# Kernel optimization log

Measured on AMD Instinct MI355X. Metric: run time of the kernel, lower is better.

Reference implementation:

```python
import jax, jax.numpy as jnp
import numpy as np

N, D, E, OUT = 100000, 128, 600000, 128


def setup_inputs() -> dict:
    key = jax.random.key(0)
    k1, k2, k3, k4, k5 = jax.random.split(key, 5)
    x = jax.random.normal(k1, (N, D), dtype=jnp.float32)
    # Linear params (stored as [in, out]; y = h @ W + b, same math as nn.Linear)
    W = jax.random.normal(k2, (D, OUT), dtype=jnp.float32) * (1.0 / np.sqrt(D))
    b = jax.random.normal(k3, (OUT,), dtype=jnp.float32) * 0.01
    # Flattened ragged neighbor lists as COO edges: node edge_dst[e] aggregates x[edge_src[e]]
    edge_src = jax.random.randint(k4, (E,), 0, N, dtype=jnp.int32)
    edge_dst = jnp.sort(jax.random.randint(k5, (E,), 0, N, dtype=jnp.int32))
    return {"x": x, "W": W, "b": b, "edge_src": edge_src, "edge_dst": edge_dst}


def reference(x, W, b, edge_src, edge_dst):
    n = x.shape[0]
    # segment-mean of neighbor features per destination node
    neigh_sum = jax.ops.segment_sum(x[edge_src], edge_dst, num_segments=n)  # [N, D]
    deg = jax.ops.segment_sum(jnp.ones((edge_dst.shape[0],), x.dtype), edge_dst, num_segments=n)  # [N]
    # nodes with no neighbors keep zero mean (matches `if neigh:` branch)
    neigh_mean = neigh_sum / jnp.maximum(deg, 1.0)[:, None]
    h = x + neigh_mean
    return jax.nn.relu(h @ W + b)
```

## Files before the change

kernel.cpp:

```cpp
#include <hip/hip_runtime.h>
#include <hip/hip_bf16.h>


#define FD  128
#define BR  32
#define BRF 64
#define HSB 136

typedef __attribute__((ext_vector_type(8))) short bf16x8;
typedef __attribute__((ext_vector_type(4))) float f32x4;

__device__ __forceinline__ short f2bf(float f) {
    unsigned u = __float_as_uint(f);
    return (short)((u + 0x7FFFu + ((u >> 16) & 1u)) >> 16);
}
__device__ __forceinline__ float bf2f(short s) {
    return __uint_as_float(((unsigned)(unsigned short)s) << 16);
}

__global__ __launch_bounds__(256) void prep_full_kernel(
    const float* __restrict__ x, const float* __restrict__ W,
    const int* __restrict__ edst, int* __restrict__ rp,
    short* __restrict__ pkW, short* __restrict__ xb, int N, int E)
{
    const int gid = blockIdx.x * 256 + threadIdx.x;
    const int nth = gridDim.x * 256;

    const int nv = N * FD / 8;
    for (int i = gid; i < nv; i += nth) {
        float4 f0 = *(const float4*)(x + (size_t)i * 8);
        float4 f1 = *(const float4*)(x + (size_t)i * 8 + 4);
        short tmp[8] = {f2bf(f0.x), f2bf(f0.y), f2bf(f0.z), f2bf(f0.w),
                        f2bf(f1.x), f2bf(f1.y), f2bf(f1.z), f2bf(f1.w)};
        *(bf16x8*)(xb + (size_t)i * 8) = *(bf16x8*)tmp;
    }
    for (int e = gid; e < E; e += nth) {
        int cur = edst[e];
        int prev = e ? edst[e - 1] : -1;
        for (int v = prev + 1; v <= cur; ++v) rp[v] = e;
        if (e == E - 1)
            for (int v = cur + 1; v <= N; ++v) rp[v] = E;
    }
    if (E == 0) {
        for (int v = gid; v <= N; v += nth) rp[v] = 0;
    }
    if (gid < 2048) {
        int wave = gid >> 9, rem = gid & 511;
        int ct = rem >> 8, rem2 = rem & 255;
        int kt = rem2 >> 6, lane = rem2 & 63;
        int q = lane >> 4, lr = lane & 15;
        int col = wave * 32 + ct * 16 + lr;
        int k0 = kt * 32 + q * 8;
        short tmp[8];
#pragma unroll
        for (int e2 = 0; e2 < 8; ++e2)
            tmp[e2] = f2bf(W[(size_t)(k0 + e2) * FD + col]);
        *(bf16x8*)(pkW + (size_t)gid * 8) = *(bf16x8*)tmp;
    }
}

__device__ __forceinline__ void issue8(const short* __restrict__ xb, int srcv,
                                       int qb, int ql, int j0, int m, uint4 v[8])
{
#pragma unroll
    for (int u = 0; u < 8; ++u) {
        int jj = j0 + u;
        int idx = __shfl(srcv, qb + (jj & 15));
        if (jj >= m) idx = 0;
        v[u] = *(const uint4*)(xb + (size_t)idx * FD + 8 * ql);
    }
}

__device__ __forceinline__ void acc8(const uint4 v[8], int c, float2 a[4])
{
#pragma unroll
    for (int u = 0; u < 8; ++u) {
        float f = (u < c) ? 1.f : 0.f;
        unsigned w;
        w = v[u].x;
        a[0].x = fmaf(__uint_as_float(w << 16), f, a[0].x);
        a[0].y = fmaf(__uint_as_float(w & 0xFFFF0000u), f, a[0].y);
        w = v[u].y;
        a[1].x = fmaf(__uint_as_float(w << 16), f, a[1].x);
        a[1].y = fmaf(__uint_as_float(w & 0xFFFF0000u), f, a[1].y);
        w = v[u].z;
        a[2].x = fmaf(__uint_as_float(w << 16), f, a[2].x);
        a[2].y = fmaf(__uint_as_float(w & 0xFFFF0000u), f, a[2].y);
        w = v[u].w;
        a[3].x = fmaf(__uint_as_float(w << 16), f, a[3].x);
        a[3].y = fmaf(__uint_as_float(w & 0xFFFF0000u), f, a[3].y);
    }
}

__device__ __forceinline__ void row_tail(const short* __restrict__ xb,
                                         const int* __restrict__ esrc,
                                         int s, int e, int srcv,
                                         int qb, int ql, float2 a[4])
{
    int deg = e - s;
    if (deg > 8) {
        uint4 v2[8];
        int m16 = deg < 16 ? deg : 16;
        issue8(xb, srcv, qb, ql, 8, m16, v2);
        acc8(v2, m16 - 8, a);
        for (int cs = s + 16; cs < e; cs += 16) {
            int m = e - cs; if (m > 16) m = 16;
            int sv = (cs + ql < e) ? esrc[cs + ql] : 0;
            for (int j0 = 0; j0 < m; j0 += 8) {
                issue8(xb, sv, qb, ql, j0, m, v2);
                int c = m - j0; if (c > 8) c = 8;
                acc8(v2, c, a);
            }
        }
    }
}

__device__ __forceinline__ void finalize_row(short* shb, int rb, int ql,
                                             const bf16x8 xv, const float2 a[4], int deg)
{
    float inv = 1.0f / (float)(deg > 0 ? deg : 1);
    short hb[8];
#pragma unroll
    for (int k = 0; k < 4; ++k) {
        hb[2 * k]     = f2bf(bf2f(xv[2 * k])     + a[k].x * inv);
        hb[2 * k + 1] = f2bf(bf2f(xv[2 * k + 1]) + a[k].y * inv);
    }
    *(bf16x8*)(shb + rb * HSB + 8 * ql) = *(bf16x8*)hb;
}

__global__ __launch_bounds__(256) void meanagg_main3_kernel(
    const short* __restrict__ xb, const short* __restrict__ pkW,
    const float* __restrict__ bias, const int* __restrict__ esrc,
    const int* __restrict__ rp, float* __restrict__ out, int N, int E)
{
    __shared__ short shb[BR * HSB];
    __shared__ int seg[BR + 1];

    const int t = threadIdx.x;
    const int base = blockIdx.x * BR;

    if (t < BR + 1) {
        int idx = base + t;
        seg[t] = rp[idx > N ? N : idx];
    }
    __syncthreads();

    const int wave = t >> 6;
    const int lane = t & 63;
    const int qw = lane >> 4;
    const int ql = lane & 15;
    const int qb = qw << 4;

    const int rb0 = wave * 8 + qw;
    const int rb1 = rb0 + 4;
    const int r0 = base + rb0, r1 = base + rb1;

    const int s0 = seg[rb0], e0 = seg[rb0 + 1];
    const int s1 = seg[rb1], e1 = seg[rb1 + 1];

    int srcv0 = (s0 + ql < e0) ? esrc[s0 + ql] : 0;
    int srcv1 = (s1 + ql < e1) ? esrc[s1 + ql] : 0;
    bf16x8 xv0 = {0, 0, 0, 0, 0, 0, 0, 0}, xv1 = xv0;
    if (r0 < N) xv0 = *(const bf16x8*)(xb + (size_t)r0 * FD + 8 * ql);
    if (r1 < N) xv1 = *(const bf16x8*)(xb + (size_t)r1 * FD + 8 * ql);

    const int deg0 = e0 - s0, deg1 = e1 - s1;
    const int m0 = deg0 < 16 ? deg0 : 16;
    const int m1 = deg1 < 16 ? deg1 : 16;

    uint4 v0[8], v1[8];
    issue8(xb, srcv0, qb, ql, 0, m0, v0);
    issue8(xb, srcv1, qb, ql, 0, m1, v1);

    float2 a[4] = {{0.f, 0.f}, {0.f, 0.f}, {0.f, 0.f}, {0.f, 0.f}};
    acc8(v0, m0 < 8 ? m0 : 8, a);
    row_tail(xb, esrc, s0, e0, srcv0, qb, ql, a);
    finalize_row(shb, rb0, ql, xv0, a, deg0);

    a[0] = a[1] = a[2] = a[3] = make_float2(0.f, 0.f);
    acc8(v1, m1 < 8 ? m1 : 8, a);
    row_tail(xb, esrc, s1, e1, srcv1, qb, ql, a);
    finalize_row(shb, rb1, ql, xv1, a, deg1);

    __syncthreads();

    const int lr = lane & 15;
    const int q  = lane >> 4;
    const int colb = wave * 32;

    bf16x8 bfr[2][4];
#pragma unroll
    for (int ct = 0; ct < 2; ++ct)
#pragma unroll
        for (int kt = 0; kt < 4; ++kt) {
            int f = ((wave * 2 + ct) * 4 + kt) * 64 + lane;
            bfr[ct][kt] = *(const bf16x8*)(pkW + (size_t)f * 8);
        }

    f32x4 acc[2][2];
#pragma unroll
    for (int rt = 0; rt < 2; ++rt) {
        acc[rt][0] = (f32x4){0.f, 0.f, 0.f, 0.f};
        acc[rt][1] = (f32x4){0.f, 0.f, 0.f, 0.f};
    }

#pragma unroll
    for (int rt = 0; rt < 2; ++rt)
#pragma unroll
        for (int kt = 0; kt < 4; ++kt) {
            bf16x8 av = *(const bf16x8*)(shb + (rt * 16 + lr) * HSB + kt * 32 + q * 8);
            acc[rt][0] = __builtin_amdgcn_mfma_f32_16x16x32_bf16(av, bfr[0][kt], acc[rt][0], 0, 0, 0);
            acc[rt][1] = __builtin_amdgcn_mfma_f32_16x16x32_bf16(av, bfr[1][kt], acc[rt][1], 0, 0, 0);
        }

    const float b0 = bias[colb + lr];
    const float b1 = bias[colb + 16 + lr];

#pragma unroll
    for (int rt = 0; rt < 2; ++rt)
#pragma unroll
        for (int j = 0; j < 4; ++j) {
            int row = base + rt * 16 + q * 4 + j;
            if (row < N) {
                float o0 = acc[rt][0][j] + b0; o0 = o0 > 0.f ? o0 : 0.f;
                float o1 = acc[rt][1][j] + b1; o1 = o1 > 0.f ? o1 : 0.f;
                out[(size_t)row * FD + colb + lr]      = o0;
                out[(size_t)row * FD + colb + 16 + lr] = o1;
            }
        }
}

__global__ __launch_bounds__(256) void prep_kernel(
    const float* __restrict__ W, const int* __restrict__ edst,
    int* __restrict__ rp, short* __restrict__ pkW, int N, int E)
{
    int gid = blockIdx.x * 256 + threadIdx.x;
    if (gid < E) {
        int cur = edst[gid];
        int prev = gid ? edst[gid - 1] : -1;
        for (int v = prev + 1; v <= cur; ++v) rp[v] = gid;
        if (gid == E - 1)
            for (int v = cur + 1; v <= N; ++v) rp[v] = E;
    }
    if (gid < 2048) {
        int wave = gid >> 9, rem = gid & 511;
        int ct = rem >> 8, rem2 = rem & 255;
        int kt = rem2 >> 6, lane = rem2 & 63;
        int q = lane >> 4, lr = lane & 15;
        int col = wave * 32 + ct * 16 + lr;
        int k0 = kt * 32 + q * 8;
        short tmp[8];
#pragma unroll
        for (int e = 0; e < 8; ++e)
            tmp[e] = f2bf(W[(size_t)(k0 + e) * FD + col]);
        *(bf16x8*)(pkW + (size_t)gid * 8) = *(bf16x8*)tmp;
    }
}

__global__ __launch_bounds__(256) void meanagg_main_kernel(
    const float* __restrict__ x, const short* __restrict__ pkW,
    const float* __restrict__ bias, const int* __restrict__ esrc,
    const int* __restrict__ rp, float* __restrict__ out, int N, int E)
{
    __shared__ short shb[BRF * HSB];
    __shared__ int seg[BRF + 1];

    const int t = threadIdx.x;
    const int base = blockIdx.x * BRF;

    if (t < BRF + 1) {
        int idx = base + t;
        seg[t] = rp[idx > N ? N : idx];
    }
    __syncthreads();

    const int wave = t >> 6;
    const int lane = t & 63;
    const int sw = lane >> 5;
    const int sl = lane & 31;
    const int lb = sw << 5;
    const int rowbase = wave * 16;

    for (int it = 0; it < 8; ++it) {
        int cur_rb = rowbase + it * 2 + sw;
        int cur_r  = base + cur_rb;
        if (cur_r >= N) break;
        int cur_s = seg[cur_rb], cur_e = seg[cur_rb + 1];
        float4 a0 = make_float4(0.f, 0.f, 0.f, 0.f), a1 = a0;
        for (int cs = cur_s; cs < cur_e; cs += 32) {
            int m = cur_e - cs; if (m > 32) m = 32;
            int srcv = (cs + sl < cur_e) ? esrc[cs + sl] : 0;
            for (int j0 = 0; j0 < m; j0 += 8) {
                const int rem = m - j0;
#pragma unroll
                for (int u = 0; u < 8; ++u) {
                    int idx = __shfl(srcv, lb + ((j0 + u) & 31));
                    float4 v = *(const float4*)(x + (size_t)idx * FD + 4 * sl);
                    float f = (u < rem) ? 1.f : 0.f;
                    float4* A = (u & 1) ? &a1 : &a0;
                    A->x = fmaf(v.x, f, A->x);
                    A->y = fmaf(v.y, f, A->y);
                    A->z = fmaf(v.z, f, A->z);
                    A->w = fmaf(v.w, f, A->w);
                }
            }
        }
        float4 xv = *(const float4*)(x + (size_t)cur_r * FD + 4 * sl);
        int deg = cur_e - cur_s;
        float inv = 1.0f / (float)(deg > 0 ? deg : 1);
        short4 hb;
        hb.x = f2bf(xv.x + (a0.x + a1.x) * inv);
        hb.y = f2bf(xv.y + (a0.y + a1.y) * inv);
        hb.z = f2bf(xv.z + (a0.z + a1.z) * inv);
        hb.w = f2bf(xv.w + (a0.w + a1.w) * inv);
        *(short4*)(shb + cur_rb * HSB + 4 * sl) = hb;
    }
    __syncthreads();

    const int lr = lane & 15;
    const int q  = lane >> 4;
    const int colb = wave * 32;

    bf16x8 bfr[2][4];
#pragma unroll
    for (int ct = 0; ct < 2; ++ct)
#pragma unroll
        for (int kt = 0; kt < 4; ++kt) {
            int f = ((wave * 2 + ct) * 4 + kt) * 64 + lane;
            bfr[ct][kt] = *(const bf16x8*)(pkW + (size_t)f * 8);
        }

    f32x4 acc[4][2];
#pragma unroll
    for (int rt = 0; rt < 4; ++rt) {
        acc[rt][0] = (f32x4){0.f, 0.f, 0.f, 0.f};
        acc[rt][1] = (f32x4){0.f, 0.f, 0.f, 0.f};
    }

#pragma unroll
    for (int rt = 0; rt < 4; ++rt)
#pragma unroll
        for (int kt = 0; kt < 4; ++kt) {
            bf16x8 av = *(const bf16x8*)(shb + (rt * 16 + lr) * HSB + kt * 32 + q * 8);
            acc[rt][0] = __builtin_amdgcn_mfma_f32_16x16x32_bf16(av, bfr[0][kt], acc[rt][0], 0, 0, 0);
            acc[rt][1] = __builtin_amdgcn_mfma_f32_16x16x32_bf16(av, bfr[1][kt], acc[rt][1], 0, 0, 0);
        }

    const float b0 = bias[colb + lr];
    const float b1 = bias[colb + 16 + lr];

#pragma unroll
    for (int rt = 0; rt < 4; ++rt)
#pragma unroll
        for (int j = 0; j < 4; ++j) {
            int row = base + rt * 16 + q * 4 + j;
            if (row < N) {
                float v0 = acc[rt][0][j] + b0; v0 = v0 > 0.f ? v0 : 0.f;
                float v1 = acc[rt][1][j] + b1; v1 = v1 > 0.f ? v1 : 0.f;
                out[(size_t)row * FD + colb + lr]      = v0;
                out[(size_t)row * FD + colb + 16 + lr] = v1;
            }
        }
}

__global__ __launch_bounds__(256) void meanagg_fused_kernel(
    const float* __restrict__ x, const float* __restrict__ W,
    const float* __restrict__ bias, const int* __restrict__ esrc,
    const int* __restrict__ edst, float* __restrict__ out, int N, int E)
{
    __shared__ short shb[BRF * HSB];
    __shared__ int seg[BRF + 1];

    const int t = threadIdx.x;
    const int base = blockIdx.x * BRF;

    if (t < BRF + 1) {
        int v = base + t;
        int lo = 0, hi = E;
        while (lo < hi) {
            int mid = (lo + hi) >> 1;
            if (edst[mid] < v) lo = mid + 1; else hi = mid;
        }
        seg[t] = lo;
    }
    __syncthreads();

    const int wave = t >> 6;
    const int lane = t & 63;
    const int sw = lane >> 5;
    const int sl = lane & 31;
    const int lb = sw << 5;
    const int rowbase = wave * 16;

    for (int it = 0; it < 8; ++it) {
        int cur_rb = rowbase + it * 2 + sw;
        int cur_r  = base + cur_rb;
        if (cur_r >= N) break;
        int cur_s = seg[cur_rb], cur_e = seg[cur_rb + 1];
        float4 a0 = make_float4(0.f, 0.f, 0.f, 0.f), a1 = a0;
        for (int cs = cur_s; cs < cur_e; cs += 32) {
            int m = cur_e - cs; if (m > 32) m = 32;
            int srcv = (cs + sl < cur_e) ? esrc[cs + sl] : 0;
            for (int j0 = 0; j0 < m; j0 += 8) {
                const int rem = m - j0;
#pragma unroll
                for (int u = 0; u < 8; ++u) {
                    int idx = __shfl(srcv, lb + ((j0 + u) & 31));
                    float4 v = *(const float4*)(x + (size_t)idx * FD + 4 * sl);
                    float f = (u < rem) ? 1.f : 0.f;
                    float4* A = (u & 1) ? &a1 : &a0;
                    A->x = fmaf(v.x, f, A->x);
                    A->y = fmaf(v.y, f, A->y);
                    A->z = fmaf(v.z, f, A->z);
                    A->w = fmaf(v.w, f, A->w);
                }
            }
        }
        float4 xv = *(const float4*)(x + (size_t)cur_r * FD + 4 * sl);
        int deg = cur_e - cur_s;
        float inv = 1.0f / (float)(deg > 0 ? deg : 1);
        short4 hb;
        hb.x = f2bf(xv.x + (a0.x + a1.x) * inv);
        hb.y = f2bf(xv.y + (a0.y + a1.y) * inv);
        hb.z = f2bf(xv.z + (a0.z + a1.z) * inv);
        hb.w = f2bf(xv.w + (a0.w + a1.w) * inv);
        *(short4*)(shb + cur_rb * HSB + 4 * sl) = hb;
    }
    __syncthreads();

    const int lr = lane & 15;
    const int q  = lane >> 4;
    const int colb = wave * 32;

    bf16x8 bfr[2][4];
#pragma unroll
    for (int ct = 0; ct < 2; ++ct) {
        int col = colb + ct * 16 + lr;
#pragma unroll
        for (int kt = 0; kt < 4; ++kt) {
            bf16x8 f;
#pragma unroll
            for (int e = 0; e < 8; ++e)
                f[e] = f2bf(W[(size_t)(kt * 32 + q * 8 + e) * FD + col]);
            bfr[ct][kt] = f;
        }
    }

    f32x4 acc[4][2];
#pragma unroll
    for (int rt = 0; rt < 4; ++rt) {
        acc[rt][0] = (f32x4){0.f, 0.f, 0.f, 0.f};
        acc[rt][1] = (f32x4){0.f, 0.f, 0.f, 0.f};
    }

#pragma unroll
    for (int rt = 0; rt < 4; ++rt)
#pragma unroll
        for (int kt = 0; kt < 4; ++kt) {
            bf16x8 av = *(const bf16x8*)(shb + (rt * 16 + lr) * HSB + kt * 32 + q * 8);
            acc[rt][0] = __builtin_amdgcn_mfma_f32_16x16x32_bf16(av, bfr[0][kt], acc[rt][0], 0, 0, 0);
            acc[rt][1] = __builtin_amdgcn_mfma_f32_16x16x32_bf16(av, bfr[1][kt], acc[rt][1], 0, 0, 0);
        }

    const float b0 = bias[colb + lr];
    const float b1 = bias[colb + 16 + lr];

#pragma unroll
    for (int rt = 0; rt < 4; ++rt)
#pragma unroll
        for (int j = 0; j < 4; ++j) {
            int row = base + rt * 16 + q * 4 + j;
            if (row < N) {
                float v0 = acc[rt][0][j] + b0; v0 = v0 > 0.f ? v0 : 0.f;
                float v1 = acc[rt][1][j] + b1; v1 = v1 > 0.f ? v1 : 0.f;
                out[(size_t)row * FD + colb + lr]      = v0;
                out[(size_t)row * FD + colb + 16 + lr] = v1;
            }
        }
}

extern "C" void kernel_launch(void* const* d_in, const int* in_sizes, int n_in,
                              void* d_out, int out_size, void* d_ws, size_t ws_size,
                              hipStream_t stream) {
    const float* x    = (const float*)d_in[0];
    const float* W    = (const float*)d_in[1];
    const float* bias = (const float*)d_in[2];
    const int* esrc   = (const int*)d_in[3];
    const int* edst   = (const int*)d_in[4];
    float* out        = (float*)d_out;

    int N = in_sizes[0] / FD;
    int E = in_sizes[3];

    size_t rp_bytes = (size_t)(N + 1) * 4;
    size_t pk_off   = (rp_bytes + 511) & ~(size_t)511;
    size_t xb_off   = (pk_off + 2048 * 8 * 2 + 511) & ~(size_t)511;
    size_t need_med = pk_off + 2048 * 8 * 2;
    size_t need_big = xb_off + (size_t)N * FD * 2;

    if (ws_size >= need_big) {
        int* rp    = (int*)d_ws;
        short* pkW = (short*)((char*)d_ws + pk_off);
        short* xb  = (short*)((char*)d_ws + xb_off);
        int blocks = (N + BR - 1) / BR;
        prep_full_kernel<<<2048, 256, 0, stream>>>(x, W, edst, rp, pkW, xb, N, E);
        meanagg_main3_kernel<<<blocks, 256, 0, stream>>>(xb, pkW, bias, esrc, rp, out, N, E);
    } else if (ws_size >= need_med) {
        int* rp    = (int*)d_ws;
        short* pkW = (short*)((char*)d_ws + pk_off);
        int blocks = (N + BRF - 1) / BRF;
        int pblocks = (E + 255) / 256;
        prep_kernel<<<pblocks, 256, 0, stream>>>(W, edst, rp, pkW, N, E);
        meanagg_main_kernel<<<blocks, 256, 0, stream>>>(x, pkW, bias, esrc, rp, out, N, E);
    } else {
        int blocks = (N + BRF - 1) / BRF;
        meanagg_fused_kernel<<<blocks, 256, 0, stream>>>(x, W, bias, esrc, edst, out, N, E);
    }
}
```

Before: 58.70 us.

## Restructure aggregation kernel to one-wave blocks over 16 rows with zero-row padding

Replaces the 256-thread, 32-row aggregation+GEMM kernel with a single-wave 64-thread kernel handling 16 rows. Each quarter-wave now processes 4 rows, with gathers software-pipelined across rows. An appended all-zero row in the bf16 copy of x replaces the per-element masking FMAs with plain adds. The epilogue computes all 128 output columns per wave with 8 MFMA tiles and uses a wave-local lgkmcnt wait instead of a block barrier. This removes barrier and shared-memory sync overhead and mask arithmetic. In exchange it reloads packed W per block and gives each wave more registers and serial work.

Result: slower. 76.04 us (+29.5%).

```diff
diff --git a/kernel.cpp b/kernel.cpp
--- a/kernel.cpp
+++ b/kernel.cpp
@@ -3,7 +3,7 @@
 
 
 #define FD  128
-#define BR  32
+#define WR  16
 #define BRF 64
 #define HSB 136
 
@@ -34,6 +34,10 @@
                         f2bf(f1.x), f2bf(f1.y), f2bf(f1.z), f2bf(f1.w)};
         *(bf16x8*)(xb + (size_t)i * 8) = *(bf16x8*)tmp;
     }
+    if (gid < 16) {
+        bf16x8 z = {0, 0, 0, 0, 0, 0, 0, 0};
+        *(bf16x8*)(xb + (size_t)N * FD + gid * 8) = z;
+    }
     for (int e = gid; e < E; e += nth) {
         int cur = edst[e];
         int prev = e ? edst[e - 1] : -1;
@@ -45,11 +49,11 @@
         for (int v = gid; v <= N; v += nth) rp[v] = 0;
     }
     if (gid < 2048) {
-        int wave = gid >> 9, rem = gid & 511;
+        int wv = gid >> 9, rem = gid & 511;
         int ct = rem >> 8, rem2 = rem & 255;
         int kt = rem2 >> 6, lane = rem2 & 63;
         int q = lane >> 4, lr = lane & 15;
-        int col = wave * 32 + ct * 16 + lr;
+        int col = wv * 32 + ct * 16 + lr;
         int k0 = kt * 32 + q * 8;
         short tmp[8];
 #pragma unroll
@@ -59,66 +63,93 @@
     }
 }
 
-__device__ __forceinline__ void issue8(const short* __restrict__ xb, int srcv,
-                                       int qb, int ql, int j0, int m, uint4 v[8])
+__device__ __forceinline__ void issue8z(const short* __restrict__ xb, int srcv,
+                                        int qb, int ql, int m, int N, uint4 v[8])
 {
 #pragma unroll
     for (int u = 0; u < 8; ++u) {
+        int idx = __shfl(srcv, qb + u);
+        if (u >= m) idx = N;
+        v[u] = *(const uint4*)(xb + (size_t)idx * FD + 8 * ql);
+    }
+}
+
+__device__ __forceinline__ void acc8z(const uint4 v[8], float2 a[4])
+{
+#pragma unroll
+    for (int u = 0; u < 8; ++u) {
+        unsigned w;
+        w = v[u].x;
+        a[0].x += __uint_as_float(w << 16);
+        a[0].y += __uint_as_float(w & 0xFFFF0000u);
+        w = v[u].y;
+        a[1].x += __uint_as_float(w << 16);
+        a[1].y += __uint_as_float(w & 0xFFFF0000u);
+        w = v[u].z;
+        a[2].x += __uint_as_float(w << 16);
+        a[2].y += __uint_as_float(w & 0xFFFF0000u);
+        w = v[u].w;
+        a[3].x += __uint_as_float(w << 16);
+        a[3].y += __uint_as_float(w & 0xFFFF0000u);
+    }
+}
+
+__device__ __forceinline__ void issue4z(const short* __restrict__ xb, int srcv,
+                                        int qb, int ql, int j0, int m, int N, uint4 v[4])
+{
+#pragma unroll
+    for (int u = 0; u < 4; ++u) {
         int jj = j0 + u;
         int idx = __shfl(srcv, qb + (jj & 15));
-        if (jj >= m) idx = 0;
+        if (jj >= m) idx = N;
         v[u] = *(const uint4*)(xb + (size_t)idx * FD + 8 * ql);
     }
 }
 
-__device__ __forceinline__ void acc8(const uint4 v[8], int c, float2 a[4])
-{
-#pragma unroll
-    for (int u = 0; u < 8; ++u) {
-        float f = (u < c) ? 1.f : 0.f;
+__device__ __forceinline__ void acc4z(const uint4 v[4], float2 a[4])
+{
+#pragma unroll
+    for (int u = 0; u < 4; ++u) {
         unsigned w;
         w = v[u].x;
-        a[0].x = fmaf(__uint_as_float(w << 16), f, a[0].x);
-        a[0].y = fmaf(__uint_as_float(w & 0xFFFF0000u), f, a[0].y);
+        a[0].x += __uint_as_float(w << 16);
+        a[0].y += __uint_as_float(w & 0xFFFF0000u);
         w = v[u].y;
-        a[1].x = fmaf(__uint_as_float(w << 16), f, a[1].x);
-        a[1].y = fmaf(__uint_as_float(w & 0xFFFF0000u), f, a[1].y);
+        a[1].x += __uint_as_float(w << 16);
+        a[1].y += __uint_as_float(w & 0xFFFF0000u);
         w = v[u].z;
-        a[2].x = fmaf(__uint_as_float(w << 16), f, a[2].x);
-        a[2].y = fmaf(__uint_as_float(w & 0xFFFF0000u), f, a[2].y);
+        a[2].x += __uint_as_float(w << 16);
+        a[2].y += __uint_as_float(w & 0xFFFF0000u);
         w = v[u].w;
-        a[3].x = fmaf(__uint_as_float(w << 16), f, a[3].x);
-        a[3].y = fmaf(__uint_as_float(w & 0xFFFF0000u), f, a[3].y);
-    }
-}
-
-__device__ __forceinline__ void row_tail(const short* __restrict__ xb,
-                                         const int* __restrict__ esrc,
-                                         int s, int e, int srcv,
-                                         int qb, int ql, float2 a[4])
+        a[3].x += __uint_as_float(w << 16);
+        a[3].y += __uint_as_float(w & 0xFFFF0000u);
+    }
+}
+
+__device__ void tailz(const short* __restrict__ xb, const int* __restrict__ esrc,
+                      int s, int e, int srcv, int qb, int ql, int N, int E, float2 a[4])
 {
     int deg = e - s;
-    if (deg > 8) {
-        uint4 v2[8];
-        int m16 = deg < 16 ? deg : 16;
-        issue8(xb, srcv, qb, ql, 8, m16, v2);
-        acc8(v2, m16 - 8, a);
-        for (int cs = s + 16; cs < e; cs += 16) {
-            int m = e - cs; if (m > 16) m = 16;
-            int sv = (cs + ql < e) ? esrc[cs + ql] : 0;
-            for (int j0 = 0; j0 < m; j0 += 8) {
-                issue8(xb, sv, qb, ql, j0, m, v2);
-                int c = m - j0; if (c > 8) c = 8;
-                acc8(v2, c, a);
-            }
-        }
-    }
-}
-
-__device__ __forceinline__ void finalize_row(short* shb, int rb, int ql,
-                                             const bf16x8 xv, const float2 a[4], int deg)
-{
-    float inv = 1.0f / (float)(deg > 0 ? deg : 1);
+    if (deg <= 8) return;
+    uint4 v2[4];
+    int m16 = deg < 16 ? deg : 16;
+    issue4z(xb, srcv, qb, ql, 8, m16, N, v2);  acc4z(v2, a);
+    issue4z(xb, srcv, qb, ql, 12, m16, N, v2); acc4z(v2, a);
+    for (int cs = s + 16; cs < e; cs += 16) {
+        int m = e - cs; if (m > 16) m = 16;
+        int ad = cs + ql; if (ad > E - 1) ad = E - 1;
+        int sv = esrc[ad];
+        for (int j0 = 0; j0 < m; j0 += 4) {
+            issue4z(xb, sv, qb, ql, j0, m, N, v2);
+            acc4z(v2, a);
+        }
+    }
+}
+
+__device__ __forceinline__ void finz(short* shb, int rb, int ql,
+                                     const bf16x8 xv, const float2 a[4], int deg)
+{
+    float inv = __builtin_amdgcn_rcpf((float)(deg > 0 ? deg : 1));
     short hb[8];
 #pragma unroll
     for (int k = 0; k < 4; ++k) {
@@ -128,106 +159,96 @@
     *(bf16x8*)(shb + rb * HSB + 8 * ql) = *(bf16x8*)hb;
 }
 
-__global__ __launch_bounds__(256) void meanagg_main3_kernel(
+__global__ __launch_bounds__(64) void meanagg_main4_kernel(
     const short* __restrict__ xb, const short* __restrict__ pkW,
     const float* __restrict__ bias, const int* __restrict__ esrc,
     const int* __restrict__ rp, float* __restrict__ out, int N, int E)
 {
-    __shared__ short shb[BR * HSB];
-    __shared__ int seg[BR + 1];
-
-    const int t = threadIdx.x;
-    const int base = blockIdx.x * BR;
-
-    if (t < BR + 1) {
-        int idx = base + t;
-        seg[t] = rp[idx > N ? N : idx];
-    }
-    __syncthreads();
-
-    const int wave = t >> 6;
-    const int lane = t & 63;
-    const int qw = lane >> 4;
-    const int ql = lane & 15;
-    const int qb = qw << 4;
-
-    const int rb0 = wave * 8 + qw;
-    const int rb1 = rb0 + 4;
-    const int r0 = base + rb0, r1 = base + rb1;
-
-    const int s0 = seg[rb0], e0 = seg[rb0 + 1];
-    const int s1 = seg[rb1], e1 = seg[rb1 + 1];
-
-    int srcv0 = (s0 + ql < e0) ? esrc[s0 + ql] : 0;
-    int srcv1 = (s1 + ql < e1) ? esrc[s1 + ql] : 0;
-    bf16x8 xv0 = {0, 0, 0, 0, 0, 0, 0, 0}, xv1 = xv0;
-    if (r0 < N) xv0 = *(const bf16x8*)(xb + (size_t)r0 * FD + 8 * ql);
-    if (r1 < N) xv1 = *(const bf16x8*)(xb + (size_t)r1 * FD + 8 * ql);
-
-    const int deg0 = e0 - s0, deg1 = e1 - s1;
-    const int m0 = deg0 < 16 ? deg0 : 16;
-    const int m1 = deg1 < 16 ? deg1 : 16;
-
-    uint4 v0[8], v1[8];
-    issue8(xb, srcv0, qb, ql, 0, m0, v0);
-    issue8(xb, srcv1, qb, ql, 0, m1, v1);
-
-    float2 a[4] = {{0.f, 0.f}, {0.f, 0.f}, {0.f, 0.f}, {0.f, 0.f}};
-    acc8(v0, m0 < 8 ? m0 : 8, a);
-    row_tail(xb, esrc, s0, e0, srcv0, qb, ql, a);
-    finalize_row(shb, rb0, ql, xv0, a, deg0);
+    __shared__ short shb[WR * HSB];
+    const int lane = threadIdx.x;
+    const int qw = lane >> 4, ql = lane & 15, qb = qw << 4;
+    const int base = blockIdx.x * WR;
+    const int rbase = base + qw * 4;
+
+    int sb[5];
+#pragma unroll
+    for (int i = 0; i < 5; ++i) {
+        int rr = rbase + i; if (rr > N) rr = N;
+        sb[i] = rp[rr];
+    }
+    const int d0 = sb[1] - sb[0], d1 = sb[2] - sb[1];
+    const int d2 = sb[3] - sb[2], d3 = sb[4] - sb[3];
+
+    int srcv[4];
+    bf16x8 xv[4];
+#pragma unroll
+    for (int i = 0; i < 4; ++i) {
+        int ad = sb[i] + ql; if (ad > E - 1) ad = E - 1; if (ad < 0) ad = 0;
+        srcv[i] = esrc[ad];
+        int rr = rbase + i; if (rr > N) rr = N;
+        xv[i] = *(const bf16x8*)(xb + (size_t)rr * FD + 8 * ql);
+    }
+
+    uint4 va[8], vb[8];
+    issue8z(xb, srcv[0], qb, ql, d0, N, va);
+    issue8z(xb, srcv[1], qb, ql, d1, N, vb);
+
+    float2 a[4];
 
     a[0] = a[1] = a[2] = a[3] = make_float2(0.f, 0.f);
-    acc8(v1, m1 < 8 ? m1 : 8, a);
-    row_tail(xb, esrc, s1, e1, srcv1, qb, ql, a);
-    finalize_row(shb, rb1, ql, xv1, a, deg1);
-
-    __syncthreads();
-
-    const int lr = lane & 15;
-    const int q  = lane >> 4;
-    const int colb = wave * 32;
-
-    bf16x8 bfr[2][4];
-#pragma unroll
-    for (int ct = 0; ct < 2; ++ct)
+    acc8z(va, a);
+    issue8z(xb, srcv[2], qb, ql, d2, N, va);
+    tailz(xb, esrc, sb[0], sb[1], srcv[0], qb, ql, N, E, a);
+    finz(shb, qw * 4 + 0, ql, xv[0], a, d0);
+
+    a[0] = a[1] = a[2] = a[3] = make_float2(0.f, 0.f);
+    acc8z(vb, a);
+    issue8z(xb, srcv[3], qb, ql, d3, N, vb);
+    tailz(xb, esrc, sb[1], sb[2], srcv[1], qb, ql, N, E, a);
+    finz(shb, qw * 4 + 1, ql, xv[1], a, d1);
+
+    a[0] = a[1] = a[2] = a[3] = make_float2(0.f, 0.f);
+    acc8z(va, a);
+    tailz(xb, esrc, sb[2], sb[3], srcv[2], qb, ql, N, E, a);
+    finz(shb, qw * 4 + 2, ql, xv[2], a, d2);
+
+    a[0] = a[1] = a[2] = a[3] = make_float2(0.f, 0.f);
+    acc8z(vb, a);
+    tailz(xb, esrc, sb[3], sb[4], srcv[3], qb, ql, N, E, a);
+    finz(shb, qw * 4 + 3, ql, xv[3], a, d3);
+
+    asm volatile("s_waitcnt lgkmcnt(0)" ::: "memory");
+
+    const int lr = lane & 15, q = lane >> 4;
+    bf16x8 af[4];
+#pragma unroll
+    for (int kt = 0; kt < 4; ++kt)
+        af[kt] = *(const bf16x8*)(shb + lr * HSB + kt * 32 + q * 8);
+
+    f32x4 oc[8];
+#pragma unroll
+    for (int nt = 0; nt < 8; ++nt) oc[nt] = (f32x4){0.f, 0.f, 0.f, 0.f};
+#pragma unroll
+    for (int nt = 0; nt < 8; ++nt)
 #pragma unroll
         for (int kt = 0; kt < 4; ++kt) {
-            int f = ((wave * 2 + ct) * 4 + kt) * 64 + lane;
-            bfr[ct][kt] = *(const bf16x8*)(pkW + (size_t)f * 8);
-        }
-
-    f32x4 acc[2][2];
-#pragma unroll
-    for (int rt = 0; rt < 2; ++rt) {
-        acc[rt][0] = (f32x4){0.f, 0.f, 0.f, 0.f};
-        acc[rt][1] = (f32x4){0.f, 0.f, 0.f, 0.f};
-    }
-
-#pragma unroll
-    for (int rt = 0; rt < 2; ++rt)
-#pragma unroll
-        for (int kt = 0; kt < 4; ++kt) {
-            bf16x8 av = *(const bf16x8*)(shb + (rt * 16 + lr) * HSB + kt * 32 + q * 8);
-            acc[rt][0] = __builtin_amdgcn_mfma_f32_16x16x32_bf16(av, bfr[0][kt], acc[rt][0], 0, 0, 0);
-            acc[rt][1] = __builtin_amdgcn_mfma_f32_16x16x32_bf16(av, bfr[1][kt], acc[rt][1], 0, 0, 0);
-        }
-
-    const float b0 = bias[colb + lr];
-    const float b1 = bias[colb + 16 + lr];
-
-#pragma unroll
-    for (int rt = 0; rt < 2; ++rt)
+            bf16x8 bf = *(const bf16x8*)(pkW + ((size_t)(nt * 4 + kt) * 64 + lane) * 8);
+            oc[nt] = __builtin_amdgcn_mfma_f32_16x16x32_bf16(af[kt], bf, oc[nt], 0, 0, 0);
+        }
+
+#pragma unroll
+    for (int nt = 0; nt < 8; ++nt) {
+        float bv = bias[nt * 16 + lr];
 #pragma unroll
         for (int j = 0; j < 4; ++j) {
-            int row = base + rt * 16 + q * 4 + j;
+            int row = base + q * 4 + j;
             if (row < N) {
-                float o0 = acc[rt][0][j] + b0; o0 = o0 > 0.f ? o0 : 0.f;
-                float o1 = acc[rt][1][j] + b1; o1 = o1 > 0.f ? o1 : 0.f;
-                out[(size_t)row * FD + colb + lr]      = o0;
-                out[(size_t)row * FD + colb + 16 + lr] = o1;
+                float v = oc[nt][j] + bv;
+                v = v > 0.f ? v : 0.f;
+                out[(size_t)row * FD + nt * 16 + lr] = v;
             }
         }
+    }
 }
 
 __global__ __launch_bounds__(256) void prep_kernel(
@@ -243,11 +264,11 @@
             for (int v = cur + 1; v <= N; ++v) rp[v] = E;
     }
     if (gid < 2048) {
-        int wave = gid >> 9, rem = gid & 511;
+        int wv = gid >> 9, rem = gid & 511;
         int ct = rem >> 8, rem2 = rem & 255;
         int kt = rem2 >> 6, lane = rem2 & 63;
         int q = lane >> 4, lr = lane & 15;
-        int col = wave * 32 + ct * 16 + lr;
+        int col = wv * 32 + ct * 16 + lr;
         int k0 = kt * 32 + q * 8;
         short tmp[8];
 #pragma unroll
@@ -305,14 +326,14 @@
                 }
             }
         }
-        float4 xv = *(const float4*)(x + (size_t)cur_r * FD + 4 * sl);
+        float4 xvv = *(const float4*)(x + (size_t)cur_r * FD + 4 * sl);
         int deg = cur_e - cur_s;
         float inv = 1.0f / (float)(deg > 0 ? deg : 1);
         short4 hb;
-        hb.x = f2bf(xv.x + (a0.x + a1.x) * inv);
-        hb.y = f2bf(xv.y + (a0.y + a1.y) * inv);
-        hb.z = f2bf(xv.z + (a0.z + a1.z) * inv);
-        hb.w = f2bf(xv.w + (a0.w + a1.w) * inv);
+        hb.x = f2bf(xvv.x + (a0.x + a1.x) * inv);
+        hb.y = f2bf(xvv.y + (a0.y + a1.y) * inv);
+        hb.z = f2bf(xvv.z + (a0.z + a1.z) * inv);
+        hb.w = f2bf(xvv.w + (a0.w + a1.w) * inv);
         *(short4*)(shb + cur_rb * HSB + 4 * sl) = hb;
     }
     __syncthreads();
@@ -416,14 +437,14 @@
                 }
             }
         }
-        float4 xv = *(const float4*)(x + (size_t)cur_r * FD + 4 * sl);
+        float4 xvv = *(const float4*)(x + (size_t)cur_r * FD + 4 * sl);
         int deg = cur_e - cur_s;
         float inv = 1.0f / (float)(deg > 0 ? deg : 1);
         short4 hb;
-        hb.x = f2bf(xv.x + (a0.x + a1.x) * inv);
-        hb.y = f2bf(xv.y + (a0.y + a1.y) * inv);
-        hb.z = f2bf(xv.z + (a0.z + a1.z) * inv);
-        hb.w = f2bf(xv.w + (a0.w + a1.w) * inv);
+        hb.x = f2bf(xvv.x + (a0.x + a1.x) * inv);
+        hb.y = f2bf(xvv.y + (a0.y + a1.y) * inv);
+        hb.z = f2bf(xvv.z + (a0.z + a1.z) * inv);
+        hb.w = f2bf(xvv.w + (a0.w + a1.w) * inv);
         *(short4*)(shb + cur_rb * HSB + 4 * sl) = hb;
     }
     __syncthreads();
@@ -496,15 +517,15 @@
     size_t pk_off   = (rp_bytes + 511) & ~(size_t)511;
     size_t xb_off   = (pk_off + 2048 * 8 * 2 + 511) & ~(size_t)511;
     size_t need_med = pk_off + 2048 * 8 * 2;
-    size_t need_big = xb_off + (size_t)N * FD * 2;
+    size_t need_big = xb_off + (size_t)(N + 1) * FD * 2;
 
     if (ws_size >= need_big) {
         int* rp    = (int*)d_ws;
         short* pkW = (short*)((char*)d_ws + pk_off);
         short* xb  = (short*)((char*)d_ws + xb_off);
-        int blocks = (N + BR - 1) / BR;
+        int blocks = (N + WR - 1) / WR;
         prep_full_kernel<<<2048, 256, 0, stream>>>(x, W, edst, rp, pkW, xb, N, E);
-        meanagg_main3_kernel<<<blocks, 256, 0, stream>>>(xb, pkW, bias, esrc, rp, out, N, E);
+        meanagg_main4_kernel<<<blocks, 64, 0, stream>>>(xb, pkW, bias, esrc, rp, out, N, E);
     } else if (ws_size >= need_med) {
         int* rp    = (int*)d_ws;
         short* pkW = (short*)((char*)d_ws + pk_off);
```
